# Optimization experiments

Hardware: AMD Instinct MI355X
Metric: run time of the kernel (lower is better)

The kernel has to match this reference:

```python
import jax, jax.numpy as jnp
import numpy as np

B, C, NMAX = 256, 1, 256   # graphs, channels, max nodes per graph
N = B * C * NMAX           # total nodes = 65536
E = N * 16                 # edges = 1,048,576
EMB, HID = 128, 128


def setup_inputs() -> dict:
    key = jax.random.key(0)
    ks = jax.random.split(key, 8)
    adj = jax.random.uniform(ks[0], (B, C, NMAX, NMAX), jnp.float32)
    edges = jax.random.randint(ks[1], (E, 2), 0, N, dtype=jnp.int32)
    subgraph_idx = jnp.repeat(jnp.arange(B, dtype=jnp.int32), C * NMAX)
    def lin(k, fan_in, fan_out):
        return jax.random.normal(k, (fan_in, fan_out), jnp.float32) / np.sqrt(fan_in).astype(np.float32)
    return {
        "adj": adj, "edges": edges, "subgraph_idx": subgraph_idx,
        "Wdec": lin(ks[2], NMAX, EMB), "bdec": jnp.zeros((EMB,), jnp.float32),
        "Wc1": lin(ks[3], EMB, HID),   "bc1": jnp.zeros((HID,), jnp.float32),
        "Wc2": lin(ks[4], HID, HID),   "bc2": jnp.zeros((HID,), jnp.float32),
        "Wp1": lin(ks[5], HID, HID),   "bp1": jnp.zeros((HID,), jnp.float32),
        "Wp2": lin(ks[6], HID, 1),     "bp2": jnp.zeros((1,), jnp.float32),
    }


def gcn_conv(x, W, b, src, dst):
    # PyG GCNConv: h = x W; add self-loops; symmetric normalization D^-1/2 (A+I) D^-1/2; + bias
    h = x @ W                                      # [N, out]
    deg = jnp.zeros((N,), x.dtype).at[dst].add(1.0) + 1.0  # in-degree incl. self loop
    dinv = jax.lax.rsqrt(deg)                      # [N]
    coef = dinv[src] * dinv[dst]                   # [E]
    agg = jax.ops.segment_sum(h[src] * coef[:, None], dst, num_segments=N)
    return agg + h * (dinv * dinv)[:, None] + b    # self-loop term + bias


def reference(adj, edges, subgraph_idx, Wdec, bdec, Wc1, bc1, Wc2, bc2, Wp1, bp1, Wp2, bp2):
    src, dst = edges[:, 0], edges[:, 1]
    # decoder_input: Linear(max_num_nodes -> embedding_dim) on flattened adjacency rows
    x = adj.reshape(-1, NMAX) @ Wdec + bdec        # [N, EMB]
    # forward applies convs[:-1] only (2 of the 3 convs); dropout is identity in eval mode
    x = jax.nn.relu(gcn_conv(x, Wc1, bc1, src, dst))
    x = jax.nn.relu(gcn_conv(x, Wc2, bc2, src, dst))
    # global max pool over nodes of each graph
    pooled = jax.ops.segment_max(x, subgraph_idx, num_segments=B)  # [B, HID]
    # post_mp MLP head
    h = jax.nn.relu(pooled @ Wp1 + bp1)
    return h @ Wp2 + bp2                           # [B, 1]
```

## Files before the change

### kernel.cpp

```cpp
#include <hip/hip_runtime.h>
#include <hip/hip_fp16.h>
#include <cstdint>
#include <cstddef>

#define NN   65536
#define NE   1048576
#define FD   128
#define KDEC 256
#define NGRAPH 256
#define DUMMY_SRC 65536u
#define EPB  4096
#define BCAP 4608
#define BCAPP 8448

typedef __attribute__((ext_vector_type(8))) short s16x8;
typedef __attribute__((ext_vector_type(4))) float f32x4;

__device__ __forceinline__ ushort f2bf(float x) {
  uint u = __float_as_uint(x);
  uint r = (u + 0x7fffu + ((u >> 16) & 1u)) >> 16;
  return (ushort)r;
}
__device__ __forceinline__ float bf2f(ushort h) {
  return __uint_as_float(((uint)h) << 16);
}

__device__ __forceinline__ void wsplit(float w, int k, int c,
                                       ushort* __restrict__ H,
                                       ushort* __restrict__ L) {
  ushort h = f2bf(w);
  size_t dst = ((size_t)((k >> 5) * 8 + (c >> 4)) * 64 +
                (size_t)((c & 15) + 16 * ((k & 31) >> 3))) * 8 + (k & 7);
  H[dst] = h;
  L[dst] = f2bf(w - bf2f(h));
}


__global__ __launch_bounds__(1024) void k_histbin(const int* __restrict__ edges,
                                                  uint* __restrict__ binbuf,
                                                  int* __restrict__ gbin,
                                                  const float* __restrict__ Wdec,
                                                  const float* __restrict__ Wc1,
                                                  const float* __restrict__ bdec,
                                                  float* __restrict__ bfused,
                                                  ushort* __restrict__ wfh,
                                                  ushort* __restrict__ wfl,
                                                  const float* __restrict__ Wc2,
                                                  ushort* __restrict__ w2h,
                                                  ushort* __restrict__ w2l) {
  const int b = blockIdx.x, t = threadIdx.x;
  if (b >= 256) {
    if (b < 288) {
      int i = (b - 256) * 1024 + t;
      int k = i >> 7, c = i & 127;
      float acc = 0.f;
#pragma unroll 8
      for (int j = 0; j < 128; j++) acc = fmaf(Wdec[k * FD + j], Wc1[j * FD + c], acc);
      wsplit(acc, k, c, wfh, wfl);
      if (b == 256 && t < 128) {
        float ba = 0.f;
        for (int j = 0; j < 128; j++) ba = fmaf(bdec[j], Wc1[j * FD + t], ba);
        bfused[t] = ba;
      }
    } else {
      int i = (b - 288) * 1024 + t;
      wsplit(Wc2[i], i >> 7, i & 127, w2h, w2l);
    }
    return;
  }
  __shared__ int lcnt[256];
  __shared__ int lsum[256];
  __shared__ int gbase[256];
  __shared__ uint sorted[EPB];

  if (t < 256) lcnt[t] = 0;
  __syncthreads();

  uint rec[4];
  ushort bkt[4], lidx[4];
#pragma unroll
  for (int r = 0; r < 4; r++) {
    int i = b * EPB + r * 1024 + t;
    int2 e = ((const int2*)edges)[i];
    int bucket = e.y >> 8;
    int li = atomicAdd(&lcnt[bucket], 1);
    rec[r] = ((uint)bucket << 24) | ((uint)(e.y & 255) << 16) | (uint)e.x;
    bkt[r] = (ushort)bucket;
    lidx[r] = (ushort)li;
  }
  __syncthreads();

  if (t < 256) lsum[t] = lcnt[t];
  __syncthreads();
  for (int off = 1; off < 256; off <<= 1) {
    int v = 0;
    if (t < 256 && t >= off) v = lsum[t - off];
    __syncthreads();
    if (t < 256) lsum[t] += v;
    __syncthreads();
  }
  if (t < 256) gbase[t] = atomicAdd(&gbin[t], lcnt[t]);
  __syncthreads();

#pragma unroll
  for (int r = 0; r < 4; r++) {
    int B = bkt[r];
    sorted[lsum[B] - lcnt[B] + lidx[r]] = rec[r];
  }
  __syncthreads();

  for (int s = t; s < EPB; s += 1024) {
    uint v = sorted[s];
    int B = v >> 24;
    int ex = lsum[B] - lcnt[B];
    binbuf[B * BCAP + gbase[B] + (s - ex)] = v & 0xFFFFFFu;
  }
}


__global__ __launch_bounds__(256) void k_misc(const uint* __restrict__ binbuf,
                                              const int* __restrict__ gbin,
                                              int* __restrict__ hist,
                                              int* __restrict__ offs,
                                              float* __restrict__ dinv,
                                              uint* __restrict__ ec) {
  __shared__ int lc[256];
  __shared__ int s[256];
  __shared__ int sofs[256];
  __shared__ int cnt2[256];
  const int b = blockIdx.x, t = threadIdx.x;
  lc[t] = 0;
  cnt2[t] = 0;
  __syncthreads();
  const int m = gbin[b];
  const uint* bp_ = binbuf + (size_t)b * BCAP;
  for (int i = t; i < m; i += 256)
    atomicAdd(&lc[bp_[i] >> 16], 1);
  __syncthreads();
  const int v = lc[t];
  const int vp = (v + 15) & ~15;
  s[t] = vp;
  __syncthreads();
  for (int off = 1; off < 256; off <<= 1) {
    int add = (t >= off) ? s[t - off] : 0;
    __syncthreads();
    s[t] += add;
    __syncthreads();
  }
  const int of = b * BCAPP + s[t] - vp;
  offs[b * 256 + t] = of;
  hist[b * 256 + t] = v;
  dinv[b * 256 + t] = rsqrtf((float)(v + 1));
  sofs[t] = of;
  __syncthreads();

  for (int i = t; i < m; i += 256) {
    uint rec = bp_[i];
    int dlow = rec >> 16;
    int pos = sofs[dlow] + atomicAdd(&cnt2[dlow], 1);
    ec[pos] = rec & 0xFFFFu;
  }
  __syncthreads();
  int base = sofs[t];
  for (int j = v; j < vp; j++) ec[base + j] = DUMMY_SRC;
}


#define GEMM_ISSUE_A(S, AR, AB)                                           \
  {                                                                       \
    _Pragma("unroll")                                                     \
    for (int mb = 0; mb < 2; mb++) {                                      \
      size_t base_ = (size_t)(r0 + mb * 16 + lr) * K + (S) * 32 + kg * 8; \
      if (AMODE == 0) {                                                   \
        const float* xp_ = (const float*)A0 + base_;                      \
        AR[mb * 2] = *(const f32x4*)xp_;                                  \
        AR[mb * 2 + 1] = *(const f32x4*)(xp_ + 4);                        \
      } else {                                                            \
        AB[mb] = *(const s16x8*)((const ushort*)A0 + base_);              \
      }                                                                   \
    }                                                                     \
  }

#define GEMM_STEP(S, AR, AB)                                              \
  {                                                                       \
    s16x8 ah[2], al[2];                                                   \
    if (AMODE == 0) {                                                     \
      _Pragma("unroll")                                                   \
      for (int mb = 0; mb < 2; mb++) {                                    \
        float xv[8] = {AR[mb*2].x, AR[mb*2].y, AR[mb*2].z, AR[mb*2].w,    \
                       AR[mb*2+1].x, AR[mb*2+1].y, AR[mb*2+1].z,          \
                       AR[mb*2+1].w};                                     \
        union { ushort u[8]; s16x8 v; } H_, L_;                           \
        _Pragma("unroll")                                                 \
        for (int e = 0; e < 8; e++) {                                     \
          ushort h_ = f2bf(xv[e]);                                        \
          H_.u[e] = h_;                                                   \
          L_.u[e] = f2bf(xv[e] - bf2f(h_));                               \
        }                                                                 \
        ah[mb] = H_.v;                                                    \
        al[mb] = L_.v;                                                    \
      }                                                                   \
    } else {                                                              \
      ah[0] = AB[0];                                                      \
      ah[1] = AB[1];                                                      \
      al[0] = AB[0];                               \
      al[1] = AB[1];                                                      \
    }                                                                     \
    if ((S) + 2 < nks) GEMM_ISSUE_A((S) + 2, AR, AB);                     \
    const bool more_ = ((S) + 1 < nks);                                   \
    if (more_) issueB((S) + 1);                                           \
    _Pragma("unroll")                                                     \
    for (int nb = 0; nb < 8; nb++) {                                      \
      s16x8 bh = *(const s16x8*)&Bs[buf][nb * 512 + l * 8];               \
      s16x8 bl = *(const s16x8*)&Bs[buf][4096 + nb * 512 + l * 8];        \
      _Pragma("unroll")                                                   \
      for (int mb = 0; mb < 2; mb++) {                                    \
        acc[mb][nb] = __builtin_amdgcn_mfma_f32_16x16x32_bf16(            \
            ah[mb], bh, acc[mb][nb], 0, 0, 0);                            \
        acc[mb][nb] = __builtin_amdgcn_mfma_f32_16x16x32_bf16(            \
            ah[mb], bl, acc[mb][nb], 0, 0, 0);                            \
        if (AMODE == 0)                                                   \
          acc[mb][nb] = __builtin_amdgcn_mfma_f32_16x16x32_bf16(          \
              al[mb], bh, acc[mb][nb], 0, 0, 0);                          \
      }                                                                   \
    }                                                                     \
    if (more_) {                                                          \
      writeB(buf ^ 1);                                                    \
      __syncthreads();                                                    \
      buf ^= 1;                                                           \
    }                                                                     \
  }

template <int AMODE>
__global__ __launch_bounds__(256) void k_gemm(const void* __restrict__ A0,
                                              const ushort* __restrict__ Whi,
                                              const ushort* __restrict__ Wlo,
                                              const float* __restrict__ bias,
                                              const float* __restrict__ scale,
                                              ushort* __restrict__ Y, int K) {
  __shared__ ushort Bs[2][8192];
  const int t = threadIdx.x;
  const int w = t >> 6;
  const int l = t & 63;
  const int lr = l & 15;
  const int kg = l >> 4;
  const int r0 = blockIdx.x * 128 + w * 32;
  const int nks = K >> 5;

  f32x4 acc[2][8];
#pragma unroll
  for (int mb = 0; mb < 2; mb++)
#pragma unroll
    for (int nb = 0; nb < 8; nb++) acc[mb][nb] = (f32x4)0.f;

  f32x4 arA[4], arB[4];
  s16x8 abA[2], abB[2];
  s16x8 bh0, bh1, bl0, bl1;

  auto issueB = [&](int s) {
    const ushort* ph = Whi + (size_t)s * 4096 + t * 16;
    const ushort* pl = Wlo + (size_t)s * 4096 + t * 16;
    bh0 = *(const s16x8*)ph;
    bh1 = *(const s16x8*)(ph + 8);
    bl0 = *(const s16x8*)pl;
    bl1 = *(const s16x8*)(pl + 8);
  };
  auto writeB = [&](int buf) {
    *(s16x8*)&Bs[buf][t * 16] = bh0;
    *(s16x8*)&Bs[buf][t * 16 + 8] = bh1;
    *(s16x8*)&Bs[buf][4096 + t * 16] = bl0;
    *(s16x8*)&Bs[buf][4096 + t * 16 + 8] = bl1;
  };

  GEMM_ISSUE_A(0, arA, abA);
  issueB(0);
  writeB(0);
  GEMM_ISSUE_A(1, arB, abB);
  __syncthreads();

  int buf = 0;
  for (int s = 0; s < nks; s += 2) {
    GEMM_STEP(s, arA, abA);
    GEMM_STEP(s + 1, arB, abB);
  }

  float dvr[2][4];
#pragma unroll
  for (int mb = 0; mb < 2; mb++)
#pragma unroll
    for (int r = 0; r < 4; r++)
      dvr[mb][r] = scale ? scale[r0 + mb * 16 + kg * 4 + r] : 1.f;

#pragma unroll
  for (int nb = 0; nb < 8; nb++) {
    int col = nb * 16 + lr;
    float bv = bias ? bias[col] : 0.f;
#pragma unroll
    for (int mb = 0; mb < 2; mb++)
#pragma unroll
      for (int r = 0; r < 4; r++) {
        size_t row = (size_t)(r0 + mb * 16 + kg * 4 + r);
        Y[row * FD + col] = f2bf((acc[mb][nb][r] + bv) * dvr[mb][r]);
      }
  }
}


template <int EMIT>
__global__ __launch_bounds__(256) void k_agg(const ushort* __restrict__ h16,
                                             const uint* __restrict__ ec,
                                             const int* __restrict__ offs,
                                             const int* __restrict__ hist,
                                             const float* __restrict__ dinv,
                                             const float* __restrict__ bias,
                                             ushort* __restrict__ yout,
                                             float* __restrict__ pooled) {
  __shared__ int pmax[128];
  const int t = threadIdx.x;
  if (EMIT == 1) {
    if (t < 128) pmax[t] = 0;
    __syncthreads();
  }
  const int n = blockIdx.x * 4 + (t >> 6);
  const int l = t & 63;
  const int half = l >> 5;
  const int dl = (l & 31) * 4;

  const int cnt_p = (hist[n] + 15) & ~15;
  const uint* ep = ec + offs[n];

  float a0 = 0.f, a1 = 0.f, a2 = 0.f, a3 = 0.f;
  float b0 = 0.f, b1 = 0.f, b2 = 0.f, b3 = 0.f;
  for (int i = half; i < cnt_p; i += 16) {
    uint s0 = ep[i];
    uint s1 = ep[i + 2];
    uint s2 = ep[i + 4];
    uint s3 = ep[i + 6];
    uint s4 = ep[i + 8];
    uint s5 = ep[i + 10];
    uint s6 = ep[i + 12];
    uint s7 = ep[i + 14];
    ushort4 v0 = *(const ushort4*)(h16 + ((size_t)s0 << 7) + dl);
    ushort4 v1 = *(const ushort4*)(h16 + ((size_t)s1 << 7) + dl);
    ushort4 v2 = *(const ushort4*)(h16 + ((size_t)s2 << 7) + dl);
    ushort4 v3 = *(const ushort4*)(h16 + ((size_t)s3 << 7) + dl);
    ushort4 v4 = *(const ushort4*)(h16 + ((size_t)s4 << 7) + dl);
    ushort4 v5 = *(const ushort4*)(h16 + ((size_t)s5 << 7) + dl);
    ushort4 v6 = *(const ushort4*)(h16 + ((size_t)s6 << 7) + dl);
    ushort4 v7 = *(const ushort4*)(h16 + ((size_t)s7 << 7) + dl);
    a0 += bf2f(v0.x); a1 += bf2f(v0.y); a2 += bf2f(v0.z); a3 += bf2f(v0.w);
    b0 += bf2f(v1.x); b1 += bf2f(v1.y); b2 += bf2f(v1.z); b3 += bf2f(v1.w);
    a0 += bf2f(v2.x); a1 += bf2f(v2.y); a2 += bf2f(v2.z); a3 += bf2f(v2.w);
    b0 += bf2f(v3.x); b1 += bf2f(v3.y); b2 += bf2f(v3.z); b3 += bf2f(v3.w);
    a0 += bf2f(v4.x); a1 += bf2f(v4.y); a2 += bf2f(v4.z); a3 += bf2f(v4.w);
    b0 += bf2f(v5.x); b1 += bf2f(v5.y); b2 += bf2f(v5.z); b3 += bf2f(v5.w);
    a0 += bf2f(v6.x); a1 += bf2f(v6.y); a2 += bf2f(v6.z); a3 += bf2f(v6.w);
    b0 += bf2f(v7.x); b1 += bf2f(v7.y); b2 += bf2f(v7.z); b3 += bf2f(v7.w);
  }
  a0 += b0; a1 += b1; a2 += b2; a3 += b3;
  a0 += __shfl_xor(a0, 32);
  a1 += __shfl_xor(a1, 32);
  a2 += __shfl_xor(a2, 32);
  a3 += __shfl_xor(a3, 32);

  if (l < 32) {
    float dv = dinv[n];
    ushort4 vs = *(const ushort4*)(h16 + ((size_t)n << 7) + dl);
    float4 bb = *(const float4*)(bias + dl);
    float o0 = fmaxf(fmaf(dv, a0 + bf2f(vs.x), bb.x), 0.f);
    float o1 = fmaxf(fmaf(dv, a1 + bf2f(vs.y), bb.y), 0.f);
    float o2 = fmaxf(fmaf(dv, a2 + bf2f(vs.z), bb.z), 0.f);
    float o3 = fmaxf(fmaf(dv, a3 + bf2f(vs.w), bb.w), 0.f);
    if (EMIT == 0) {
      ushort4 hi;
      hi.x = f2bf(o0);
      hi.y = f2bf(o1);
      hi.z = f2bf(o2);
      hi.w = f2bf(o3);
      *(ushort4*)(yout + (size_t)n * FD + dl) = hi;
    } else {
      atomicMax(&pmax[dl + 0], __float_as_int(o0));
      atomicMax(&pmax[dl + 1], __float_as_int(o1));
      atomicMax(&pmax[dl + 2], __float_as_int(o2));
      atomicMax(&pmax[dl + 3], __float_as_int(o3));
    }
  }
  if (EMIT == 1) {
    __syncthreads();
    if (t < 128) {
      int gr = blockIdx.x >> 6;
      atomicMax((int*)pooled + gr * FD + t, pmax[t]);
    }
  }
}


__global__ __launch_bounds__(128) void k_mlp(const float* __restrict__ pooled,
                                             const float* __restrict__ Wp1,
                                             const float* __restrict__ bp1,
                                             const float* __restrict__ Wp2,
                                             const float* __restrict__ bp2,
                                             float* __restrict__ out) {
  __shared__ float row[128];
  __shared__ float red[128];
  int g = blockIdx.x, t = threadIdx.x;
  row[t] = pooled[g * FD + t];
  __syncthreads();
  float acc = bp1[t];
#pragma unroll 8
  for (int k = 0; k < 128; k++) acc = fmaf(row[k], Wp1[k * FD + t], acc);
  acc = fmaxf(acc, 0.f);
  red[t] = acc * Wp2[t];
  __syncthreads();
  for (int st = 64; st > 0; st >>= 1) {
    if (t < st) red[t] += red[t + st];
    __syncthreads();
  }
  if (t == 0) out[g] = red[0] + bp2[0];
}


extern "C" void kernel_launch(void* const* d_in, const int* in_sizes, int n_in,
                              void* d_out, int out_size, void* d_ws, size_t ws_size,
                              hipStream_t stream) {
  (void)in_sizes; (void)n_in; (void)out_size; (void)ws_size;

  const float* adj  = (const float*)d_in[0];
  const int*   edges= (const int*)d_in[1];
  const float* Wdec = (const float*)d_in[3];
  const float* bdec = (const float*)d_in[4];
  const float* Wc1  = (const float*)d_in[5];
  const float* bc1  = (const float*)d_in[6];
  const float* Wc2  = (const float*)d_in[7];
  const float* bc2  = (const float*)d_in[8];
  const float* Wp1  = (const float*)d_in[9];
  const float* bp1  = (const float*)d_in[10];
  const float* Wp2  = (const float*)d_in[11];
  const float* bp2  = (const float*)d_in[12];
  float* out = (float*)d_out;

  char* ws = (char*)d_ws;
  size_t off = 0;
  auto alloc = [&](size_t bytes) -> void* {
    void* p = ws + off;
    off += (bytes + 255) & ~(size_t)255;
    return p;
  };
  ushort* h16  = (ushort*)alloc((size_t)(NN + 1) * FD * 2);
  ushort* x1   = (ushort*)alloc((size_t)NN * FD * 2);
  float*  pooled = (float*)alloc((size_t)NGRAPH * FD * 4);
  int*    gbin = (int*)alloc(256 * 4);
  int*    hist = (int*)alloc((size_t)NN * 4);
  int*    offs = (int*)alloc((size_t)NN * 4);
  uint*   ec   = (uint*)alloc((size_t)256 * BCAPP * 4);
  uint*   binbuf = (uint*)alloc((size_t)256 * BCAP * 4);
  float*  dinv = (float*)alloc((size_t)NN * 4);
  float*  bfused = (float*)alloc(FD * 4);
  ushort* wfh = (ushort*)alloc((size_t)KDEC * FD * 2);
  ushort* wfl = (ushort*)alloc((size_t)KDEC * FD * 2);
  ushort* w2h = (ushort*)alloc((size_t)FD * FD * 2);
  ushort* w2l = (ushort*)alloc((size_t)FD * FD * 2);

  hipMemsetAsync(pooled, 0, (size_t)NGRAPH * FD * 4 + 256 * 4, stream);
  hipMemsetAsync(h16 + (size_t)NN * FD, 0, FD * 2, stream);

  k_histbin<<<304, 1024, 0, stream>>>(edges, binbuf, gbin, Wdec, Wc1, bdec,
                                      bfused, wfh, wfl, Wc2, w2h, w2l);
  k_misc<<<256, 256, 0, stream>>>(binbuf, gbin, hist, offs, dinv, ec);

  k_gemm<0><<<NN / 128, 256, 0, stream>>>(adj, wfh, wfl, bfused, dinv, h16, KDEC);

  k_agg<0><<<NN / 4, 256, 0, stream>>>(h16, ec, offs, hist, dinv, bc1, x1, nullptr);

  k_gemm<1><<<NN / 128, 256, 0, stream>>>(x1, w2h, w2l, nullptr, dinv, h16, FD);

  k_agg<1><<<NN / 4, 256, 0, stream>>>(h16, ec, offs, hist, dinv, bc2, nullptr, pooled);

  k_mlp<<<NGRAPH, 128, 0, stream>>>(pooled, Wp1, bp1, Wp2, bp2, out);
}
```

Baseline: 167.6 us.

## Slice node features into four 32-column planes for cache-friendly gather aggregation

The GEMM now writes its output into four column slices, each a contiguous table of 64-byte rows. The aggregation kernel runs one block per slice per group of four nodes, launching four times as many blocks. Each wave gathers only a 32-column slice across eight edge lanes, so each gather working set is a quarter of the full feature table and fits better in L2/MALL. Edge-list padding drops from 16 to 8 to reduce wasted dummy gathers. The costs are re-reading the edge lists four times, more shuffle reductions, and more blocks doing pooling atomics.

```diff
diff --git a/kernel.cpp b/kernel.cpp
--- a/kernel.cpp
+++ b/kernel.cpp
@@ -11,7 +11,8 @@
 #define DUMMY_SRC 65536u
 #define EPB  4096
 #define BCAP 4608
-#define BCAPP 8448
+#define BCAPP 6656
+#define SLROW (NN + 1)
 
 typedef __attribute__((ext_vector_type(8))) short s16x8;
 typedef __attribute__((ext_vector_type(4))) float f32x4;
@@ -123,7 +124,8 @@
                                               int* __restrict__ hist,
                                               int* __restrict__ offs,
                                               float* __restrict__ dinv,
-                                              uint* __restrict__ ec) {
+                                              uint* __restrict__ ec,
+                                              ushort* __restrict__ h16s) {
   __shared__ int lc[256];
   __shared__ int s[256];
   __shared__ int sofs[256];
@@ -138,7 +140,7 @@
     atomicAdd(&lc[bp_[i] >> 16], 1);
   __syncthreads();
   const int v = lc[t];
-  const int vp = (v + 15) & ~15;
+  const int vp = (v + 7) & ~7;
   s[t] = vp;
   __syncthreads();
   for (int off = 1; off < 256; off <<= 1) {
@@ -163,6 +165,10 @@
   __syncthreads();
   int base = sofs[t];
   for (int j = v; j < vp; j++) ec[base + j] = DUMMY_SRC;
+  if (b == 0 && t < 128) {
+    int sl = t >> 5, d = t & 31;
+    h16s[((size_t)sl * SLROW + NN) * 32 + d] = 0;
+  }
 }
 
 
@@ -295,78 +301,72 @@
   for (int nb = 0; nb < 8; nb++) {
     int col = nb * 16 + lr;
     float bv = bias ? bias[col] : 0.f;
+    size_t sbase = (size_t)(col >> 5) * SLROW * 32 + (col & 31);
 #pragma unroll
     for (int mb = 0; mb < 2; mb++)
 #pragma unroll
       for (int r = 0; r < 4; r++) {
         size_t row = (size_t)(r0 + mb * 16 + kg * 4 + r);
-        Y[row * FD + col] = f2bf((acc[mb][nb][r] + bv) * dvr[mb][r]);
+        Y[sbase + row * 32] = f2bf((acc[mb][nb][r] + bv) * dvr[mb][r]);
       }
   }
 }
 
 
 template <int EMIT>
-__global__ __launch_bounds__(256) void k_agg(const ushort* __restrict__ h16,
+__global__ __launch_bounds__(256) void k_agg(const ushort* __restrict__ h16s,
                                              const uint* __restrict__ ec,
                                              const int* __restrict__ offs,
                                              const int* __restrict__ hist,
                                              const float* __restrict__ dinv,
                                              const float* __restrict__ bias,
-                                             ushort* __restrict__ yout,
+                                             ushort* __restrict__ x1,
                                              float* __restrict__ pooled) {
-  __shared__ int pmax[128];
-  const int t = threadIdx.x;
+  __shared__ int pmax[32];
+  const int bid = blockIdx.x, t = threadIdx.x;
+  const int s = bid & 3;
+  const int n = (bid >> 2) * 4 + (t >> 6);
+  const int l = t & 63;
+  const int p = l >> 3;
+  const int q = l & 7;
   if (EMIT == 1) {
-    if (t < 128) pmax[t] = 0;
-    __syncthreads();
-  }
-  const int n = blockIdx.x * 4 + (t >> 6);
-  const int l = t & 63;
-  const int half = l >> 5;
-  const int dl = (l & 31) * 4;
-
-  const int cnt_p = (hist[n] + 15) & ~15;
+    if (t < 32) pmax[t] = 0;
+    __syncthreads();
+  }
+
+  const ushort* tab = h16s + (size_t)s * SLROW * 32 + q * 4;
+  const int cnt_p = (hist[n] + 7) & ~7;
   const uint* ep = ec + offs[n];
 
   float a0 = 0.f, a1 = 0.f, a2 = 0.f, a3 = 0.f;
   float b0 = 0.f, b1 = 0.f, b2 = 0.f, b3 = 0.f;
-  for (int i = half; i < cnt_p; i += 16) {
+  int i = p;
+  for (; i + 8 < cnt_p; i += 16) {
     uint s0 = ep[i];
-    uint s1 = ep[i + 2];
-    uint s2 = ep[i + 4];
-    uint s3 = ep[i + 6];
-    uint s4 = ep[i + 8];
-    uint s5 = ep[i + 10];
-    uint s6 = ep[i + 12];
-    uint s7 = ep[i + 14];
-    ushort4 v0 = *(const ushort4*)(h16 + ((size_t)s0 << 7) + dl);
-    ushort4 v1 = *(const ushort4*)(h16 + ((size_t)s1 << 7) + dl);
-    ushort4 v2 = *(const ushort4*)(h16 + ((size_t)s2 << 7) + dl);
-    ushort4 v3 = *(const ushort4*)(h16 + ((size_t)s3 << 7) + dl);
-    ushort4 v4 = *(const ushort4*)(h16 + ((size_t)s4 << 7) + dl);
-    ushort4 v5 = *(const ushort4*)(h16 + ((size_t)s5 << 7) + dl);
-    ushort4 v6 = *(const ushort4*)(h16 + ((size_t)s6 << 7) + dl);
-    ushort4 v7 = *(const ushort4*)(h16 + ((size_t)s7 << 7) + dl);
+    uint s1 = ep[i + 8];
+    ushort4 v0 = *(const ushort4*)(tab + (size_t)s0 * 32);
+    ushort4 v1 = *(const ushort4*)(tab + (size_t)s1 * 32);
     a0 += bf2f(v0.x); a1 += bf2f(v0.y); a2 += bf2f(v0.z); a3 += bf2f(v0.w);
     b0 += bf2f(v1.x); b1 += bf2f(v1.y); b2 += bf2f(v1.z); b3 += bf2f(v1.w);
-    a0 += bf2f(v2.x); a1 += bf2f(v2.y); a2 += bf2f(v2.z); a3 += bf2f(v2.w);
-    b0 += bf2f(v3.x); b1 += bf2f(v3.y); b2 += bf2f(v3.z); b3 += bf2f(v3.w);
-    a0 += bf2f(v4.x); a1 += bf2f(v4.y); a2 += bf2f(v4.z); a3 += bf2f(v4.w);
-    b0 += bf2f(v5.x); b1 += bf2f(v5.y); b2 += bf2f(v5.z); b3 += bf2f(v5.w);
-    a0 += bf2f(v6.x); a1 += bf2f(v6.y); a2 += bf2f(v6.z); a3 += bf2f(v6.w);
-    b0 += bf2f(v7.x); b1 += bf2f(v7.y); b2 += bf2f(v7.z); b3 += bf2f(v7.w);
+  }
+  if (i < cnt_p) {
+    uint s0 = ep[i];
+    ushort4 v0 = *(const ushort4*)(tab + (size_t)s0 * 32);
+    a0 += bf2f(v0.x); a1 += bf2f(v0.y); a2 += bf2f(v0.z); a3 += bf2f(v0.w);
   }
   a0 += b0; a1 += b1; a2 += b2; a3 += b3;
-  a0 += __shfl_xor(a0, 32);
-  a1 += __shfl_xor(a1, 32);
-  a2 += __shfl_xor(a2, 32);
-  a3 += __shfl_xor(a3, 32);
-
-  if (l < 32) {
+#pragma unroll
+  for (int m = 8; m <= 32; m <<= 1) {
+    a0 += __shfl_xor(a0, m);
+    a1 += __shfl_xor(a1, m);
+    a2 += __shfl_xor(a2, m);
+    a3 += __shfl_xor(a3, m);
+  }
+
+  if (p == 0) {
     float dv = dinv[n];
-    ushort4 vs = *(const ushort4*)(h16 + ((size_t)n << 7) + dl);
-    float4 bb = *(const float4*)(bias + dl);
+    ushort4 vs = *(const ushort4*)(tab + (size_t)n * 32);
+    float4 bb = *(const float4*)(bias + s * 32 + q * 4);
     float o0 = fmaxf(fmaf(dv, a0 + bf2f(vs.x), bb.x), 0.f);
     float o1 = fmaxf(fmaf(dv, a1 + bf2f(vs.y), bb.y), 0.f);
     float o2 = fmaxf(fmaf(dv, a2 + bf2f(vs.z), bb.z), 0.f);
@@ -377,19 +377,19 @@
       hi.y = f2bf(o1);
       hi.z = f2bf(o2);
       hi.w = f2bf(o3);
-      *(ushort4*)(yout + (size_t)n * FD + dl) = hi;
+      *(ushort4*)(x1 + (size_t)n * FD + s * 32 + q * 4) = hi;
     } else {
-      atomicMax(&pmax[dl + 0], __float_as_int(o0));
-      atomicMax(&pmax[dl + 1], __float_as_int(o1));
-      atomicMax(&pmax[dl + 2], __float_as_int(o2));
-      atomicMax(&pmax[dl + 3], __float_as_int(o3));
+      atomicMax(&pmax[q * 4 + 0], __float_as_int(o0));
+      atomicMax(&pmax[q * 4 + 1], __float_as_int(o1));
+      atomicMax(&pmax[q * 4 + 2], __float_as_int(o2));
+      atomicMax(&pmax[q * 4 + 3], __float_as_int(o3));
     }
   }
   if (EMIT == 1) {
     __syncthreads();
-    if (t < 128) {
-      int gr = blockIdx.x >> 6;
-      atomicMax((int*)pooled + gr * FD + t, pmax[t]);
+    if (t < 32) {
+      int gr = bid >> 8;
+      atomicMax((int*)pooled + gr * FD + s * 32 + t, pmax[t]);
     }
   }
 }
@@ -446,7 +446,7 @@
     off += (bytes + 255) & ~(size_t)255;
     return p;
   };
-  ushort* h16  = (ushort*)alloc((size_t)(NN + 1) * FD * 2);
+  ushort* h16s = (ushort*)alloc((size_t)4 * SLROW * 32 * 2);
   ushort* x1   = (ushort*)alloc((size_t)NN * FD * 2);
   float*  pooled = (float*)alloc((size_t)NGRAPH * FD * 4);
   int*    gbin = (int*)alloc(256 * 4);
@@ -462,19 +462,18 @@
   ushort* w2l = (ushort*)alloc((size_t)FD * FD * 2);
 
   hipMemsetAsync(pooled, 0, (size_t)NGRAPH * FD * 4 + 256 * 4, stream);
-  hipMemsetAsync(h16 + (size_t)NN * FD, 0, FD * 2, stream);
 
   k_histbin<<<304, 1024, 0, stream>>>(edges, binbuf, gbin, Wdec, Wc1, bdec,
                                       bfused, wfh, wfl, Wc2, w2h, w2l);
-  k_misc<<<256, 256, 0, stream>>>(binbuf, gbin, hist, offs, dinv, ec);
-
-  k_gemm<0><<<NN / 128, 256, 0, stream>>>(adj, wfh, wfl, bfused, dinv, h16, KDEC);
-
-  k_agg<0><<<NN / 4, 256, 0, stream>>>(h16, ec, offs, hist, dinv, bc1, x1, nullptr);
-
-  k_gemm<1><<<NN / 128, 256, 0, stream>>>(x1, w2h, w2l, nullptr, dinv, h16, FD);
-
-  k_agg<1><<<NN / 4, 256, 0, stream>>>(h16, ec, offs, hist, dinv, bc2, nullptr, pooled);
+  k_misc<<<256, 256, 0, stream>>>(binbuf, gbin, hist, offs, dinv, ec, h16s);
+
+  k_gemm<0><<<NN / 128, 256, 0, stream>>>(adj, wfh, wfl, bfused, dinv, h16s, KDEC);
+
+  k_agg<0><<<NN, 256, 0, stream>>>(h16s, ec, offs, hist, dinv, bc1, x1, nullptr);
+
+  k_gemm<1><<<NN / 128, 256, 0, stream>>>(x1, w2h, w2l, nullptr, dinv, h16s, FD);
+
+  k_agg<1><<<NN, 256, 0, stream>>>(h16s, ec, offs, hist, dinv, bc2, nullptr, pooled);
 
   k_mlp<<<NGRAPH, 128, 0, stream>>>(pooled, Wp1, bp1, Wp2, bp2, out);
 }
```

Result: slower. 250.3 us (+49.3%).
